# Optimization experiments

Hardware: AMD Instinct MI355X
Metric: run time of the kernel (lower is better)

Reference implementation:

```python
import jax, jax.numpy as jnp
import numpy as np

B, N, C_IN = 2048, 62, 512
NUM_LAYERS, H, C_OUT_PER_HEAD = 3, 8, 64


def setup_inputs() -> dict:
    key = jax.random.key(0)
    k1, k2, k3, k4 = jax.random.split(key, 4)
    x = jax.random.normal(k1, (B, N, C_IN), dtype=jnp.float32)
    L = jax.random.uniform(k2, (N, N), dtype=jnp.float32)
    W_alphas = jax.random.normal(k3, (NUM_LAYERS, H, C_IN, N), dtype=jnp.float32) * 0.05
    W = jax.random.normal(k4, (NUM_LAYERS, H, C_IN, C_OUT_PER_HEAD), dtype=jnp.float32) * 0.05
    return {"x": x, "L": L, "W_alphas": W_alphas, "W": W}


def reference(x, L, W_alphas, W):
    # x: [B, N, C]; L: [N, N]; W_alphas: [Lyr, H, C, N]; W: [Lyr, H, C, Co]
    num_layers = W_alphas.shape[0]
    n = x.shape[1]
    I = jnp.eye(n, dtype=x.dtype)
    # Chebyshev-style adjacency powers: [I, L, L@L, ...]
    adjs = [I, L]
    for _ in range(2, num_layers):
        adjs.append(adjs[-1] @ L)
    adjs = adjs[:num_layers]

    result = None
    for l in range(num_layers):
        A = adjs[l]
        A_hat = A + I
        D = A.sum(axis=-1)                      # [N]
        d_neg = jnp.where(D == 0, 0.0, 1.0 / D)  # torch: D^-1 with inf -> 0
        # attention logits per head: D_neg @ (x @ W_alphas[h]) -> [H, B, N, N]
        a = jnp.einsum('bnc,hcm->hbnm', x, W_alphas[l])
        a = d_neg[:, None] * a                   # diag(D_neg) @ M == row scaling
        a = jax.nn.leaky_relu(a, 0.01)
        a = jax.nn.softmax(a, axis=-2)           # softmax over rows (dim=-2)
        ax = jnp.einsum('nm,bmc->bnc', A_hat, x)  # A_hat @ x, shared across heads
        o = jnp.einsum('hbnm,bmc->hbnc', a, ax)
        o = jnp.einsum('hbnc,hco->hbno', o, W[l])
        o = jax.nn.relu(o)
        # concat heads along feature dim (head-major order, matching torch.cat)
        o = jnp.moveaxis(o, 0, 2).reshape(o.shape[1], n, -1)  # [B, N, H*Co]
        result = o if result is None else result + o
    return jax.nn.relu(result)
```

## Files before the change

kernel.cpp:

```cpp
#include <hip/hip_runtime.h>


using f32x4 = __attribute__((ext_vector_type(4))) float;
using s16x8 = __attribute__((ext_vector_type(8))) short;

__device__ __forceinline__ unsigned short f2bf(float f){
  unsigned int u = __builtin_bit_cast(unsigned int, f);
  u += 0x7fffu + ((u >> 16) & 1u);
  return (unsigned short)(u >> 16);
}
__device__ __forceinline__ float bf2f(unsigned short h){
  unsigned int u = ((unsigned int)h) << 16;
  return __builtin_bit_cast(float, u);
}
__device__ __forceinline__ f32x4 zf4(){ f32x4 v; v[0]=0.f; v[1]=0.f; v[2]=0.f; v[3]=0.f; return v; }

__device__ __forceinline__ void async16(const void* g, void* l){
  __builtin_amdgcn_global_load_lds((const __attribute__((address_space(1))) unsigned int*)g,
                                   (__attribute__((address_space(3))) unsigned int*)l,
                                   16, 0, 0);
}

__global__ void k_prep_adj(const float* __restrict__ L,
                           unsigned short* __restrict__ ahat,
                           float* __restrict__ dneg)
{
  __shared__ float Ls[62*62];
  __shared__ float A2s[62*62];
  const int tid = threadIdx.x;
  for (int i = tid; i < 62*62; i += 256) Ls[i] = L[i];
  __syncthreads();
  for (int i = tid; i < 62*62; i += 256){
    const int n = i / 62, m = i % 62;
    float s = 0.f;
    for (int k = 0; k < 62; ++k) s += Ls[n*62 + k] * Ls[k*62 + m];
    A2s[i] = s;
  }
  __syncthreads();
  for (int i = tid; i < 3*64*64; i += 256){
    const int l = i >> 12, r = i & 4095, n = r >> 6, m = r & 63;
    float v = 0.f;
    if (n < 62 && m < 62){
      float base = 0.f;
      if (l == 0) base = (n == m) ? 1.f : 0.f;
      else if (l == 1) base = Ls[n*62 + m];
      else base = A2s[n*62 + m];
      v = base + ((n == m) ? 1.f : 0.f);
    }
    ahat[i] = f2bf(v);
  }
  for (int i = tid; i < 3*64; i += 256){
    const int l = i >> 6, n = i & 63;
    float D = 0.f;
    if (n < 62){
      if (l == 0) D = 1.f;
      else {
        const float* src = (l == 1) ? Ls : A2s;
        for (int m = 0; m < 62; ++m) D += src[n*62 + m];
      }
    }
    dneg[i] = (D == 0.f) ? 0.f : 1.f / D;
  }
}

__global__ void k_prep_w(const float* __restrict__ Wa, const float* __restrict__ W,
                         unsigned short* __restrict__ WaT, unsigned short* __restrict__ WT)
{
  const int idx = blockIdx.x * 256 + threadIdx.x;
  if (idx < 786432){
    const int c = idx & 511, m = (idx >> 9) & 63, lh = idx >> 15;
    const float v = (m < 62) ? Wa[((size_t)lh*512 + c)*62 + m] : 0.f;
    WaT[idx] = f2bf(v);
  } else if (idx < 1572864){
    const int j = idx - 786432;
    const int c = j & 511, o = (j >> 9) & 63, lh = j >> 15;
    WT[j] = f2bf(W[((size_t)lh*512 + c)*64 + o]);
  }
}

#define LP 72

__global__ __launch_bounds__(256, 2)
void k_main(const float* __restrict__ x,
            const unsigned short* __restrict__ WaT,
            const unsigned short* __restrict__ WT,
            const unsigned short* __restrict__ ahat,
            const float* __restrict__ dneg,
            float* __restrict__ out)
{
  __shared__ __align__(16) unsigned short s_chunk[2][8192];
  __shared__ __align__(16) unsigned short s_a[64*LP];
  __shared__ __align__(16) unsigned short s_xwT[64*LP];
  __shared__ __align__(16) unsigned short s_axwT[64*LP];
  __shared__ __align__(16) float s_dneg[192];
  __shared__ __align__(16) float s_red[256];
  __shared__ __align__(16) float s_red2[256];

  const int tid  = threadIdx.x;
  const int wv   = tid >> 6;
  const int lane = tid & 63;
  const int q    = lane >> 4;
  const int m15  = lane & 15;
  const int b    = blockIdx.x;
  const int r0   = 16*wv + 4*q;

  if (tid < 192) s_dneg[tid] = dneg[tid];

  s16x8 afr[16];
  {
    const int row = 16*wv + m15;
    if (row < 62){
      const float* xp = x + ((size_t)b*62 + row)*512 + q*8;
      #pragma unroll
      for (int kk = 0; kk < 16; ++kk){
        const f32x4 f0 = *(const f32x4*)(xp + kk*32);
        const f32x4 f1 = *(const f32x4*)(xp + kk*32 + 4);
        s16x8 t;
        t[0]=(short)f2bf(f0[0]); t[1]=(short)f2bf(f0[1]); t[2]=(short)f2bf(f0[2]); t[3]=(short)f2bf(f0[3]);
        t[4]=(short)f2bf(f1[0]); t[5]=(short)f2bf(f1[1]); t[6]=(short)f2bf(f1[2]); t[7]=(short)f2bf(f1[3]);
        afr[kk] = t;
      }
    } else {
      #pragma unroll
      for (int kk = 0; kk < 16; ++kk){
        s16x8 t; t[0]=0;t[1]=0;t[2]=0;t[3]=0;t[4]=0;t[5]=0;t[6]=0;t[7]=0; afr[kk] = t;
      }
    }
  }

  #pragma unroll 1
  for (int h = 0; h < 8; ++h){
    f32x4 out_acc[4];
    #pragma unroll
    for (int ct = 0; ct < 4; ++ct) out_acc[ct] = zf4();

    #pragma unroll 1
    for (int l = 0; l < 3; ++l){
      const int lh = l*8 + h;
      const unsigned short* wa_base = WaT + (size_t)lh*32768;
      const unsigned short* wt_base = WT  + (size_t)lh*32768;

      f32x4 accL[4], accX[4];
      #pragma unroll
      for (int ct = 0; ct < 4; ++ct){ accL[ct] = zf4(); accX[ct] = zf4(); }

      #pragma unroll
      for (int kc = 0; kc < 4; ++kc){
        __syncthreads();
        #pragma unroll
        for (int tt = 0; tt < 4; ++tt){
          const int n  = 16*tt + 4*wv + q;
          const int jl = m15 ^ (n & 15);
          const size_t goff = (size_t)n*512 + (size_t)kc*128 + (size_t)jl*8;
          const int    loff = tt*2048 + wv*512 + lane*8;
          async16(wa_base + goff, &s_chunk[0][loff]);
          async16(wt_base + goff, &s_chunk[1][loff]);
        }
        __syncthreads();
        #pragma unroll
        for (int ks = 0; ks < 4; ++ks){
          const s16x8 a = afr[kc*4 + ks];
          #pragma unroll
          for (int ct = 0; ct < 4; ++ct){
            const int off = (16*ct + m15)*128 + (((4*ks + q) ^ m15) * 8);
            const s16x8 bL = *(const s16x8*)(&s_chunk[0][off]);
            const s16x8 bX = *(const s16x8*)(&s_chunk[1][off]);
            accL[ct] = __builtin_amdgcn_mfma_f32_16x16x32_bf16(a, bL, accL[ct], 0, 0, 0);
            accX[ct] = __builtin_amdgcn_mfma_f32_16x16x32_bf16(a, bX, accX[ct], 0, 0, 0);
          }
        }
      }

      {
        const f32x4 dn = *(const f32x4*)(&s_dneg[l*64 + r0]);
        #pragma unroll
        for (int ct = 0; ct < 4; ++ct){
          const int col = 16*ct + m15;
          #pragma unroll
          for (int r = 0; r < 4; ++r){
            const int n = r0 + r;
            float v = accL[ct][r] * dn[r];
            v = (v > 0.f) ? v : 0.01f*v;
            if (n >= 62) v = -1e30f;
            s_a[n*LP + col]   = f2bf(v);
            s_xwT[col*LP + n] = f2bf(accX[ct][r]);
          }
        }
      }
      __syncthreads();

      f32x4 accA[4];
      #pragma unroll
      for (int ct = 0; ct < 4; ++ct) accA[ct] = zf4();
      #pragma unroll
      for (int ks = 0; ks < 2; ++ks){
        const s16x8 aA = *(const s16x8*)(ahat + (size_t)(l*64 + 16*wv + m15)*64 + ks*32 + q*8);
        #pragma unroll
        for (int ct = 0; ct < 4; ++ct){
          const s16x8 bA = *(const s16x8*)(&s_xwT[(16*ct + m15)*LP + ks*32 + q*8]);
          accA[ct] = __builtin_amdgcn_mfma_f32_16x16x32_bf16(aA, bA, accA[ct], 0, 0, 0);
        }
      }
      #pragma unroll
      for (int ct = 0; ct < 4; ++ct){
        #pragma unroll
        for (int r = 0; r < 4; ++r)
          s_axwT[(16*ct + m15)*LP + (r0 + r)] = f2bf(accA[ct][r]);
      }

      float vsm[16];
      float mp = -3.0e38f;
      #pragma unroll
      for (int i = 0; i < 16; ++i){
        vsm[i] = bf2f(s_a[(16*wv + i)*LP + lane]);
        mp = fmaxf(mp, vsm[i]);
      }
      s_red[wv*64 + lane] = mp;
      __syncthreads();
      const float mc = fmaxf(fmaxf(s_red[lane], s_red[64 + lane]),
                             fmaxf(s_red[128 + lane], s_red[192 + lane]));
      float ev[16]; float sp = 0.f;
      #pragma unroll
      for (int i = 0; i < 16; ++i){ ev[i] = __expf(vsm[i] - mc); sp += ev[i]; }
      s_red2[wv*64 + lane] = sp;
      __syncthreads();
      const float sc = s_red2[lane] + s_red2[64 + lane] + s_red2[128 + lane] + s_red2[192 + lane];
      const float inv = 1.0f / sc;
      #pragma unroll
      for (int i = 0; i < 16; ++i)
        s_a[(16*wv + i)*LP + lane] = f2bf(ev[i] * inv);
      __syncthreads();

      f32x4 accO[4];
      #pragma unroll
      for (int ct = 0; ct < 4; ++ct) accO[ct] = zf4();
      #pragma unroll
      for (int ks = 0; ks < 2; ++ks){
        const s16x8 aO = *(const s16x8*)(&s_a[(16*wv + m15)*LP + ks*32 + q*8]);
        #pragma unroll
        for (int ct = 0; ct < 4; ++ct){
          const s16x8 bO = *(const s16x8*)(&s_axwT[(16*ct + m15)*LP + ks*32 + q*8]);
          accO[ct] = __builtin_amdgcn_mfma_f32_16x16x32_bf16(aO, bO, accO[ct], 0, 0, 0);
        }
      }
      #pragma unroll
      for (int ct = 0; ct < 4; ++ct){
        #pragma unroll
        for (int r = 0; r < 4; ++r)
          out_acc[ct][r] += fmaxf(accO[ct][r], 0.f);
      }
    }

    #pragma unroll
    for (int ct = 0; ct < 4; ++ct){
      const int col = h*64 + 16*ct + m15;
      #pragma unroll
      for (int r = 0; r < 4; ++r){
        const int n = r0 + r;
        if (n < 62)
          out[((size_t)b*62 + n)*512 + col] = fmaxf(out_acc[ct][r], 0.f);
      }
    }
  }
}

extern "C" void kernel_launch(void* const* d_in, const int* in_sizes, int n_in,
                              void* d_out, int out_size, void* d_ws, size_t ws_size,
                              hipStream_t stream)
{
  const float* x  = (const float*)d_in[0];
  const float* L  = (const float*)d_in[1];
  const float* Wa = (const float*)d_in[2];
  const float* W  = (const float*)d_in[3];
  float* out = (float*)d_out;

  char* ws = (char*)d_ws;
  unsigned short* ws_ahat = (unsigned short*)(ws);
  float*          ws_dneg = (float*)(ws + 24576);
  unsigned short* ws_WaT  = (unsigned short*)(ws + 25600);
  unsigned short* ws_WT   = (unsigned short*)(ws + 25600 + 1572864);

  k_prep_adj<<<1, 256, 0, stream>>>(L, ws_ahat, ws_dneg);
  k_prep_w<<<6144, 256, 0, stream>>>(Wa, W, ws_WaT, ws_WT);
  k_main<<<2048, 256, 0, stream>>>(x, ws_WaT, ws_WT, ws_ahat, ws_dneg, out);
}
```

Measured before the change: 1.042 ms.

## Double-buffer weight staging into LDS and overlap async loads with MFMA

```diff
diff --git a/kernel.cpp b/kernel.cpp
--- a/kernel.cpp
+++ b/kernel.cpp
@@ -88,13 +88,14 @@
             const float* __restrict__ dneg,
             float* __restrict__ out)
 {
-  __shared__ __align__(16) unsigned short s_chunk[2][8192];
-  __shared__ __align__(16) unsigned short s_a[64*LP];
-  __shared__ __align__(16) unsigned short s_xwT[64*LP];
-  __shared__ __align__(16) unsigned short s_axwT[64*LP];
+  __shared__ __align__(16) unsigned short s_u[16384];
   __shared__ __align__(16) float s_dneg[192];
   __shared__ __align__(16) float s_red[256];
   __shared__ __align__(16) float s_red2[256];
+
+  unsigned short* const s_a    = s_u;
+  unsigned short* const s_xwT  = s_u + 4608;
+  unsigned short* const s_axwT = s_u + 9216;
 
   const int tid  = threadIdx.x;
   const int wv   = tid >> 6;
@@ -106,6 +107,9 @@
 
   if (tid < 192) s_dneg[tid] = dneg[tid];
 
+  const int srow = lane >> 3;
+  const int sseg = (lane & 7) ^ srow;
+
   s16x8 afr[16];
   {
     const int row = 16*wv + m15;
@@ -140,35 +144,47 @@
       const unsigned short* wa_base = WaT + (size_t)lh*32768;
       const unsigned short* wt_base = WT  + (size_t)lh*32768;
 
+      auto STAGE = [&](int kc, int bufsel){
+        unsigned short* const lb = s_u + bufsel*8192;
+        #pragma unroll
+        for (int s = 0; s < 4; ++s){
+          const int n = (s & 1)*32 + wv*8 + srow;
+          const unsigned short* gb = (s < 2) ? wa_base : wt_base;
+          const int loff = ((s < 2) ? 0 : 4096) + (s & 1)*2048 + wv*512 + lane*8;
+          async16(gb + (size_t)n*512 + kc*64 + sseg*8, lb + loff);
+        }
+      };
+
       f32x4 accL[4], accX[4];
       #pragma unroll
       for (int ct = 0; ct < 4; ++ct){ accL[ct] = zf4(); accX[ct] = zf4(); }
 
-      #pragma unroll
-      for (int kc = 0; kc < 4; ++kc){
-        __syncthreads();
-        #pragma unroll
-        for (int tt = 0; tt < 4; ++tt){
-          const int n  = 16*tt + 4*wv + q;
-          const int jl = m15 ^ (n & 15);
-          const size_t goff = (size_t)n*512 + (size_t)kc*128 + (size_t)jl*8;
-          const int    loff = tt*2048 + wv*512 + lane*8;
-          async16(wa_base + goff, &s_chunk[0][loff]);
-          async16(wt_base + goff, &s_chunk[1][loff]);
-        }
-        __syncthreads();
-        #pragma unroll
-        for (int ks = 0; ks < 4; ++ks){
-          const s16x8 a = afr[kc*4 + ks];
+      __syncthreads();
+      STAGE(0, 0);
+      asm volatile("s_waitcnt vmcnt(0)" ::: "memory");
+      __builtin_amdgcn_s_barrier();
+      __builtin_amdgcn_sched_barrier(0);
+
+      #pragma unroll
+      for (int kc = 0; kc < 8; ++kc){
+        if (kc < 7) STAGE(kc + 1, (kc + 1) & 1);
+        const unsigned short* bw = s_u + (kc & 1)*8192;
+        #pragma unroll
+        for (int ks = 0; ks < 2; ++ks){
+          const s16x8 a = afr[kc*2 + ks];
           #pragma unroll
           for (int ct = 0; ct < 4; ++ct){
-            const int off = (16*ct + m15)*128 + (((4*ks + q) ^ m15) * 8);
-            const s16x8 bL = *(const s16x8*)(&s_chunk[0][off]);
-            const s16x8 bX = *(const s16x8*)(&s_chunk[1][off]);
+            const int off = (16*ct + m15)*64 + (((4*ks + q) ^ (m15 & 7)) * 8);
+            const s16x8 bL = *(const s16x8*)(bw + off);
+            const s16x8 bX = *(const s16x8*)(bw + 4096 + off);
             accL[ct] = __builtin_amdgcn_mfma_f32_16x16x32_bf16(a, bL, accL[ct], 0, 0, 0);
             accX[ct] = __builtin_amdgcn_mfma_f32_16x16x32_bf16(a, bX, accX[ct], 0, 0, 0);
           }
         }
+        __builtin_amdgcn_sched_barrier(0);
+        asm volatile("s_waitcnt vmcnt(0)" ::: "memory");
+        __builtin_amdgcn_s_barrier();
+        __builtin_amdgcn_sched_barrier(0);
       }
 
       {
```

New measurement: 1.245 ms. +19.5%, slower.
